# Optimization experiments

Measured on AMD Instinct MI355X. Metric: run time of the kernel, lower is better.

Reference implementation:

```python
import jax, jax.numpy as jnp
import numpy as np

NUM_CLASSES = 3
POS_T, NEG_T = 0.5, 0.3
RATIO = 3
W_OBJ, W_CLS, W_LOC = 1.0, 1.0, 2.0


def _pairwise_iou(a, b):
    # a: [N,4] anchors, b: [G,4] gt boxes, xyxy
    ix1 = jnp.maximum(a[:, None, 0], b[None, :, 0])
    iy1 = jnp.maximum(a[:, None, 1], b[None, :, 1])
    ix2 = jnp.minimum(a[:, None, 2], b[None, :, 2])
    iy2 = jnp.minimum(a[:, None, 3], b[None, :, 3])
    inter = jnp.clip(ix2 - ix1, 0) * jnp.clip(iy2 - iy1, 0)
    area_a = (a[:, 2] - a[:, 0]) * (a[:, 3] - a[:, 1])
    area_b = (b[:, 2] - b[:, 0]) * (b[:, 3] - b[:, 1])
    union = area_a[:, None] + area_b[None, :] - inter
    return inter / jnp.maximum(union, 1e-9)


def _masked_mean(x, m):
    c = m.sum()
    return jnp.where(c > 0, (x * m).sum() / jnp.maximum(c, 1.0), 0.0)


def _per_image(pred, anc, ax, ay, aw, ah, boxes_gt, labels_gt):
    # pred: [N, 5+nc]; anc: [N,4]; boxes_gt: [G,4]; labels_gt: [G] in 1..nc
    iou = _pairwise_iou(anc, boxes_gt)              # [N, G]
    best = jnp.argmax(iou, axis=1)
    best_iou = jnp.max(iou, axis=1)
    pos = best_iou >= POS_T
    neg = best_iou < NEG_T
    mb = boxes_gt[best]                             # matched boxes [N,4]
    ml = labels_gt[best]                            # matched labels [N]
    obj_logit = pred[:, 4]
    cls_logit = pred[:, 5:]
    obj_t = pos.astype(pred.dtype)
    # BCEWithLogits (numerically stable)
    obj_loss = jnp.maximum(obj_logit, 0) - obj_logit * obj_t + jnp.log1p(jnp.exp(-jnp.abs(obj_logit)))
    # hard negative mining: top-(3*num_pos) detached obj losses among negatives
    num_pos = pos.sum()
    k = jnp.minimum(RATIO * num_pos, neg.sum())
    cand = jnp.where(neg, jax.lax.stop_gradient(obj_loss), -1.0)
    order = jnp.argsort(-cand)
    ranks = jnp.zeros_like(order).at[order].set(jnp.arange(order.shape[0], dtype=order.dtype))
    sel_neg = neg & (ranks < k)
    loss_obj = _masked_mean(obj_loss, (pos | sel_neg).astype(pred.dtype))
    # classification over positives, labels shifted to 0-based
    logp = jax.nn.log_softmax(cls_logit, axis=-1)
    tgt = jnp.clip(ml - 1, 0)
    ce = -jnp.take_along_axis(logp, tgt[:, None], axis=1)[:, 0]
    loss_cls = _masked_mean(ce, pos.astype(pred.dtype))
    # localization over positives: SmoothL1 on encoded offsets
    gx = (mb[:, 0] + mb[:, 2]) * 0.5
    gy = (mb[:, 1] + mb[:, 3]) * 0.5
    gw = jnp.maximum(mb[:, 2] - mb[:, 0], 1e-6)
    gh = jnp.maximum(mb[:, 3] - mb[:, 1], 1e-6)
    loc_tgt = jnp.stack([(gx - ax) / aw, (gy - ay) / ah,
                         jnp.log(gw / aw), jnp.log(gh / ah)], axis=1)
    d = pred[:, :4] - loc_tgt
    ad = jnp.abs(d)
    sl1 = jnp.where(ad < 1.0, 0.5 * d * d, ad - 0.5)  # [N,4]
    pm = pos.astype(pred.dtype)
    cnt = 4.0 * pm.sum()
    loss_loc = jnp.where(cnt > 0, (sl1 * pm[:, None]).sum() / jnp.maximum(cnt, 1.0), 0.0)
    return loss_obj, loss_cls, loss_loc


def _detection_loss(preds, ancs, gt_boxes, gt_labels):
    B = preds[0].shape[0]
    obj_s = 0.0
    cls_s = 0.0
    loc_s = 0.0
    for pred, anc in zip(preds, ancs):
        Bp, C, H, W = pred.shape
        p = jnp.transpose(pred, (0, 2, 3, 1)).reshape(Bp, -1, 5 + NUM_CLASSES)
        ax = (anc[:, 0] + anc[:, 2]) * 0.5
        ay = (anc[:, 1] + anc[:, 3]) * 0.5
        aw = jnp.maximum(anc[:, 2] - anc[:, 0], 1e-6)
        ah = jnp.maximum(anc[:, 3] - anc[:, 1], 1e-6)
        lo, lc, ll = jax.vmap(
            lambda pb, bb, lb: _per_image(pb, anc, ax, ay, aw, ah, bb, lb)
        )(p, gt_boxes, gt_labels)
        obj_s = obj_s + lo.sum()
        cls_s = cls_s + lc.sum()
        loc_s = loc_s + ll.sum()
    obj_m = obj_s / B
    cls_m = cls_s / B
    loc_m = loc_s / B
    total = W_OBJ * obj_m + W_CLS * cls_m + W_LOC * loc_m
    return total, obj_m, cls_m, loc_m


def setup_inputs() -> dict:
    key = jax.random.key(0)
    k = jax.random.split(key, 8)
    B, G, A = 32, 50, 3
    img = 512.0
    scales = [(128, 128), (64, 64), (32, 32)]
    C = A * (5 + NUM_CLASSES)  # 24

    def make_anchors(H, W):
        stride = img / H
        ys, xs = np.meshgrid(np.arange(H), np.arange(W), indexing="ij")
        cx = (xs + 0.5) * stride
        cy = (ys + 0.5) * stride
        per = []
        for s in (1.0, 1.5, 2.0):
            half = s * stride
            per.append(np.stack([cx - half, cy - half, cx + half, cy + half], axis=-1).reshape(-1, 4))
        b = np.stack(per, axis=1).reshape(-1, 4)  # [H*W*A, 4], A innermost
        return jnp.asarray(b, dtype=jnp.float32)

    preds = [jax.random.normal(k[i], (B, C, H, W), dtype=jnp.float32) for i, (H, W) in enumerate(scales)]
    ancs = [make_anchors(H, W) for (H, W) in scales]
    cx = jax.random.uniform(k[3], (B, G)) * 384.0 + 64.0
    cy = jax.random.uniform(k[4], (B, G)) * 384.0 + 64.0
    w = jax.random.uniform(k[5], (B, G)) * 112.0 + 16.0
    h = jax.random.uniform(k[6], (B, G)) * 112.0 + 16.0
    gt_boxes = jnp.stack([cx - w / 2, cy - h / 2, cx + w / 2, cy + h / 2], axis=-1).astype(jnp.float32)
    gt_labels = jax.random.randint(k[7], (B, G), 1, NUM_CLASSES + 1)
    return {"p0": preds[0], "p1": preds[1], "p2": preds[2],
            "a0": ancs[0], "a1": ancs[1], "a2": ancs[2],
            "gt_boxes": gt_boxes, "gt_labels": gt_labels}


def reference(p0, p1, p2, a0, a1, a2, gt_boxes, gt_labels):
    return _detection_loss([p0, p1, p2], [a0, a1, a2], gt_boxes, gt_labels)
```

## Files before the change

### kernel.cpp

```cpp
#include <hip/hip_runtime.h>

#define SLOT_U64     200
#define NBLOCKS      2688
#define NBINS        192
#define BIN_OFF      872
#define SUM_SCALE    33554432.0f
#define INV_SUM_SCALE (1.0f/33554432.0f)

__device__ __forceinline__ float sl1f(float d){
  float ad = fabsf(d); return ad < 1.f ? 0.5f*d*d : ad - 0.5f;
}

__global__ __launch_bounds__(256) void k_main(
    const float* __restrict__ p0, const float* __restrict__ p1, const float* __restrict__ p2,
    const float* __restrict__ gtb, const int* __restrict__ gtl,
    unsigned long long* __restrict__ ws64)
{
  const int id = blockIdx.x;
  int s, bIm, chunk, H, lw; const float* p;
  if (id < 2048){ s=0; H=128; lw=7; chunk=id>>5;            bIm=id&31;          p=p0; }
  else if (id < 2560){ s=1; H=64; lw=6; chunk=(id-2048)>>5; bIm=(id-2048)&31;   p=p1; }
  else {              s=2; H=32; lw=5; chunk=(id-2560)>>5;  bIm=(id-2560)&31;   p=p2; }
  const int W = H, HW = H*W;
  const float stride = 512.0f/(float)H;
  const int tid = threadIdx.x;

  __shared__ float4 sBox[52];
  __shared__ float  sArea[52], sGx[52], sGy[52], sGw[52], sGh[52];
  __shared__ int    sLbl[52];
  __shared__ int    sNk;
  __shared__ unsigned long long sH[NBINS];
  __shared__ float  sRF[3][4];
  __shared__ unsigned int sRU[4];

  if (tid < 64){
    const int ymin = (chunk*256)>>lw;
    const int rowc = 256>>lw;
    const float by1 = ((float)ymin+0.5f)*stride - 2.0f*stride;
    const float by2 = ((float)(ymin+rowc-1)+0.5f)*stride + 2.0f*stride;
    bool keep=false; float4 gb=make_float4(0,0,0,0); int lbl=0;
    if (tid < 50){
      gb  = *(const float4*)(gtb + ((size_t)bIm*50 + tid)*4);
      lbl = gtl[bIm*50 + tid];
      keep = (fminf(by2, gb.w) - fmaxf(by1, gb.y)) > 0.f;
    }
    unsigned long long m = __ballot(keep);
    if (keep){
      int idx = __popcll(m & ((1ull<<tid)-1ull));
      sBox[idx]=gb;
      sArea[idx]=(gb.z-gb.x)*(gb.w-gb.y);
      sGx[idx]=(gb.x+gb.z)*0.5f;  sGy[idx]=(gb.y+gb.w)*0.5f;
      sGw[idx]=fmaxf(gb.z-gb.x,1e-6f); sGh[idx]=fmaxf(gb.w-gb.y,1e-6f);
      sLbl[idx]=lbl;
    }
    if (tid==0) sNk = __popcll(m);
  }
  if (tid < NBINS) sH[tid]=0ull;
  __syncthreads();

  const int nk = sNk;
  const int hw  = chunk*256 + tid;
  const int hwW = chunk*256 + (tid & ~63);
  const int y = hw>>lw, x = hw&(W-1);
  const float cx = ((float)x+0.5f)*stride, cy = ((float)y+0.5f)*stride;

  const float* pb = p + (size_t)bIm*24*HW + hw;
  float xo[3];
  #pragma unroll
  for (int a=0;a<3;a++) xo[a] = pb[(size_t)(a*8+4)*HW];

  const int wxlo = (W >= 64) ? (hwW & (W-1)) : 0;
  const int wxhi = (W >= 64) ? (wxlo + 63)   : (W-1);
  const int wylo = hwW>>lw, wyhi = (hwW+63)>>lw;
  const float m2 = 2.0f*stride;
  const float wx1 = ((float)wxlo+0.5f)*stride - m2;
  const float wx2 = ((float)wxhi+0.5f)*stride + m2;
  const float wy1 = ((float)wylo+0.5f)*stride - m2;
  const float wy2 = ((float)wyhi+0.5f)*stride + m2;

  float half[3]; half[0]=stride; half[1]=1.5f*stride; half[2]=2.0f*stride;
  float areaA[3], bi[3], bu[3]; int bj[3];
  #pragma unroll
  for (int a=0;a<3;a++){
    const float aw = 2.0f*half[a];
    areaA[a]=aw*aw; bi[a]=0.f; bu[a]=1e-9f; bj[a]=0;
  }
  for (int j=0;j<nk;j++){
    const float4 gb = sBox[j];
    if (gb.x >= wx2 || gb.z <= wx1 || gb.y >= wy2 || gb.w <= wy1) continue;
    const float ar = sArea[j];
    #pragma unroll
    for (int a=0;a<3;a++){
      const float iy1 = fmaxf(cy-half[a], gb.y), iy2 = fminf(cy+half[a], gb.w);
      const float ih  = fmaxf(iy2-iy1, 0.f);
      const float ix1 = fmaxf(cx-half[a], gb.x), ix2 = fminf(cx+half[a], gb.z);
      const float iw  = fmaxf(ix2-ix1, 0.f);
      const float inter = iw*ih;
      const float un = areaA[a] + ar - inter;
      if (inter*bu[a] > bi[a]*un){ bi[a]=inter; bu[a]=un; bj[a]=j; }
    }
  }

  int accPN=0;
  float accObj=0.f, accCls=0.f, accLoc=0.f;
  #pragma unroll
  for (int a=0;a<3;a++){
    const bool pos = bi[a] >= 0.5f*bu[a];
    const bool neg = bi[a] < 0.3f*bu[a];
    if (pos || neg){
      float objl = fmaxf(xo[a],0.f) - (pos ? xo[a] : 0.f)
                 + __logf(1.f + __expf(-fabsf(xo[a])));
      objl = fmaxf(objl, 0.f);
      if (neg){
        accPN += (1<<16);
        const int bin = min(max((int)(__float_as_uint(objl)>>20) - BIN_OFF, 0), NBINS-1);
        const unsigned long long pack =
            (1ull<<48) | (unsigned long long)__float2uint_rn(objl * SUM_SCALE);
        atomicAdd(&sH[bin], pack);
      } else {
        accPN += 1; accObj += objl;
        const int jb = bj[a];
        const float aw = 2.0f*half[a];
        const float c0=pb[(size_t)(a*8+5)*HW], c1=pb[(size_t)(a*8+6)*HW], c2=pb[(size_t)(a*8+7)*HW];
        const float mm = fmaxf(fmaxf(c0,c1),c2);
        const float lse = mm + __logf(__expf(c0-mm)+__expf(c1-mm)+__expf(c2-mm));
        const int t = max(sLbl[jb]-1, 0);
        const float ct = (t==0)?c0 : (t==1)?c1 : c2;
        accCls += lse - ct;
        const float tx = (sGx[jb]-cx)/aw;
        const float ty = (sGy[jb]-cy)/aw;
        const float tw = __logf(sGw[jb]/aw);
        const float th = __logf(sGh[jb]/aw);
        accLoc += sl1f(pb[(size_t)(a*8+0)*HW]-tx) + sl1f(pb[(size_t)(a*8+1)*HW]-ty)
                + sl1f(pb[(size_t)(a*8+2)*HW]-tw) + sl1f(pb[(size_t)(a*8+3)*HW]-th);
      }
    }
  }

  #pragma unroll
  for (int o=32;o;o>>=1){
    accPN  += __shfl_down(accPN,o,64);
    accObj += __shfl_down(accObj,o,64);
    accCls += __shfl_down(accCls,o,64);
    accLoc += __shfl_down(accLoc,o,64);
  }
  if ((tid & 63)==0){
    const int w = tid>>6;
    sRU[w]=(unsigned)accPN;
    sRF[0][w]=accObj; sRF[1][w]=accCls; sRF[2][w]=accLoc;
  }
  __syncthreads();

  unsigned long long* slot = ws64 + (size_t)id*SLOT_U64;
  if (tid < NBINS) slot[tid] = sH[tid];
  if (tid==0){
    unsigned t=0; float ob=0,cl=0,lc=0;
    #pragma unroll
    for (int w=0;w<4;w++){ t+=sRU[w]; ob+=sRF[0][w]; cl+=sRF[1][w]; lc+=sRF[2][w]; }
    slot[192] = ((unsigned long long)(t & 0xFFFFu) << 32) | (unsigned long long)(t >> 16);
    slot[193] = (unsigned long long)__float_as_uint(ob);
    slot[194] = (unsigned long long)__float_as_uint(cl);
    slot[195] = (unsigned long long)__float_as_uint(lc);
  }
}

__global__ __launch_bounds__(256) void k_select(const unsigned long long* __restrict__ ws64,
                                                float* __restrict__ out){
  const int g = blockIdx.x, tid = threadIdx.x;
  const int s = g>>5, bIm = g&31;
  const int nb   = (s==0)?64:(s==1)?16:4;
  const int base = (s==0)?0:(s==1)?2048:2560;

  __shared__ unsigned long long sHm[NBINS];
  __shared__ unsigned int sPos, sNeg;
  __shared__ float sObj, sCls, sLoc;

  if (tid < NBINS){
    unsigned long long a0=0ull, a1=0ull;
    int b=0;
    for (; b+1<nb; b+=2){
      a0 += ws64[(size_t)(base + b*32 + bIm)*SLOT_U64 + tid];
      a1 += ws64[(size_t)(base + (b+1)*32 + bIm)*SLOT_U64 + tid];
    }
    if (b<nb) a0 += ws64[(size_t)(base + b*32 + bIm)*SLOT_U64 + tid];
    sHm[tid] = a0 + a1;
  } else if (tid < 196){
    const int j = tid - 192;
    if (j==0){
      unsigned long long t=0ull;
      for (int b=0;b<nb;b++) t += ws64[(size_t)(base + b*32 + bIm)*SLOT_U64 + 192];
      sPos = (unsigned)(t>>32); sNeg = (unsigned)(t & 0xFFFFFFFFull);
    } else {
      float f=0.f;
      for (int b=0;b<nb;b++)
        f += __uint_as_float((unsigned)ws64[(size_t)(base + b*32 + bIm)*SLOT_U64 + 192 + j]);
      if (j==1) sObj=f; else if (j==2) sCls=f; else sLoc=f;
    }
  }
  __syncthreads();
  if (tid >= 64) return;

  const int lane = tid;
  const int pos  = (int)sPos;
  const int negc = (int)sNeg;
  const int k = min(3*pos, negc);
  float selSum = 0.f;

  if (k > 0){
    unsigned int c[3]; float sm[3];
    #pragma unroll
    for (int j=0;j<3;j++){
      const unsigned long long d = sHm[lane*3+j];
      c[j]  = (unsigned int)(d>>48);
      sm[j] = (float)(d & 0xFFFFFFFFFFFFull) * INV_SUM_SCALE;
    }
    const unsigned int c3 = c[0]+c[1]+c[2];
    unsigned int incl = c3;
    #pragma unroll
    for (int off=1; off<64; off<<=1){
      unsigned int yv = __shfl_down(incl, off, 64);
      if (lane+off < 64) incl += yv;
    }
    const unsigned int excl = incl - c3;
    int   tieL = -1, rL = 0; float avgL = 0.f;
    const bool hit = (excl < (unsigned)k) && (incl >= (unsigned)k);
    if (hit){
      unsigned int cum = excl;
      #pragma unroll
      for (int j=2;j>=0;j--){
        const unsigned int cc = c[j];
        if (cum + cc >= (unsigned)k){
          tieL = lane*3+j; rL = (int)((unsigned)k - cum);
          avgL = sm[j]/(float)cc;
          break;
        }
        cum += cc;
      }
    }
    const unsigned long long hm = __ballot(hit);
    const int src = __ffsll((long long)hm) - 1;
    const int   tie = __shfl(tieL, src, 64);
    const int   r   = __shfl(rL,   src, 64);
    const float avg = __shfl(avgL, src, 64);
    float above = 0.f;
    #pragma unroll
    for (int j=0;j<3;j++) if (lane*3+j > tie) above += sm[j];
    #pragma unroll
    for (int o=32;o;o>>=1) above += __shfl_down(above,o,64);
    selSum = above + (float)r * avg;
  }
  if (lane==0){
    const int cObj = pos + k;
    const float lo = (cObj>0) ? (sObj+selSum)/(float)cObj : 0.f;
    const float lc = (pos>0)  ? sCls/(float)pos           : 0.f;
    const float ll = (pos>0)  ? sLoc/(float)(4*pos)       : 0.f;
    const float invB = 1.f/32.f;
    atomicAdd(out+0, (lo + lc + 2.f*ll)*invB);
    atomicAdd(out+1, lo*invB);
    atomicAdd(out+2, lc*invB);
    atomicAdd(out+3, ll*invB);
  }
}

extern "C" void kernel_launch(void* const* d_in, const int* in_sizes, int n_in,
                              void* d_out, int out_size, void* d_ws, size_t ws_size,
                              hipStream_t stream){
  if (ws_size < (size_t)NBLOCKS*SLOT_U64*8) return;
  const float* p0  = (const float*)d_in[0];
  const float* p1  = (const float*)d_in[1];
  const float* p2  = (const float*)d_in[2];
  const float* gtb = (const float*)d_in[6];
  const int*   gtl = (const int*)d_in[7];
  unsigned long long* ws64 = (unsigned long long*)d_ws;
  float* out = (float*)d_out;

  hipLaunchKernelGGL(k_main,   dim3(NBLOCKS), dim3(256), 0, stream, p0,p1,p2,gtb,gtl,ws64);
  hipLaunchKernelGGL(k_select, dim3(96),      dim3(256), 0, stream, ws64, out);
}
```

Baseline: 141.2 us.

## Process four rows per thread to cut block count and reuse x-overlap math

Each main-kernel block now covers 1024 anchor positions instead of 256, with each thread handling four rows spaced 256 positions apart. The x-direction intersection is computed once per GT box and reused across the four rows. This cuts block count by four, along with per-block GT filtering, histogram init and slot writes, and the number of slots k_select must reduce, whose loop is unrolled by four. The costs are a looser per-wave GT culling window (taller y-range, so more boxes are tested), more registers per thread, and fewer blocks to fill the GPU.

```diff
diff --git a/kernel.cpp b/kernel.cpp
--- a/kernel.cpp
+++ b/kernel.cpp
@@ -1,7 +1,7 @@
 #include <hip/hip_runtime.h>
 
 #define SLOT_U64     200
-#define NBLOCKS      2688
+#define NBLOCKS      672
 #define NBINS        192
 #define BIN_OFF      872
 #define SUM_SCALE    33554432.0f
@@ -18,9 +18,9 @@
 {
   const int id = blockIdx.x;
   int s, bIm, chunk, H, lw; const float* p;
-  if (id < 2048){ s=0; H=128; lw=7; chunk=id>>5;            bIm=id&31;          p=p0; }
-  else if (id < 2560){ s=1; H=64; lw=6; chunk=(id-2048)>>5; bIm=(id-2048)&31;   p=p1; }
-  else {              s=2; H=32; lw=5; chunk=(id-2560)>>5;  bIm=(id-2560)&31;   p=p2; }
+  if (id < 512){      s=0; H=128; lw=7; chunk=id>>5;         bIm=id&31;        p=p0; }
+  else if (id < 640){ s=1; H=64;  lw=6; chunk=(id-512)>>5;   bIm=(id-512)&31;  p=p1; }
+  else {              s=2; H=32;  lw=5; chunk=0;             bIm=(id-640)&31;  p=p2; }
   const int W = H, HW = H*W;
   const float stride = 512.0f/(float)H;
   const int tid = threadIdx.x;
@@ -33,9 +33,25 @@
   __shared__ float  sRF[3][4];
   __shared__ unsigned int sRU[4];
 
+  const int hw0 = chunk*1024 + tid;
+  const int y0 = hw0>>lw, x = hw0&(W-1);
+  const float cx  = ((float)x+0.5f)*stride;
+  const float dy  = (float)(256>>lw)*stride;
+  float cyr[4];
+  cyr[0] = ((float)y0+0.5f)*stride;
+  cyr[1] = cyr[0]+dy; cyr[2] = cyr[0]+2.f*dy; cyr[3] = cyr[0]+3.f*dy;
+
+  const float* pb = p + (size_t)bIm*24*HW + hw0;
+  float xo[4][3];
+  #pragma unroll
+  for (int a=0;a<3;a++){
+    #pragma unroll
+    for (int r=0;r<4;r++) xo[r][a] = pb[(size_t)(a*8+4)*HW + r*256];
+  }
+
   if (tid < 64){
-    const int ymin = (chunk*256)>>lw;
-    const int rowc = 256>>lw;
+    const int ymin = (chunk*1024)>>lw;
+    const int rowc = 1024>>lw;
     const float by1 = ((float)ymin+0.5f)*stride - 2.0f*stride;
     const float by2 = ((float)(ymin+rowc-1)+0.5f)*stride + 2.0f*stride;
     bool keep=false; float4 gb=make_float4(0,0,0,0); int lbl=0;
@@ -59,19 +75,11 @@
   __syncthreads();
 
   const int nk = sNk;
-  const int hw  = chunk*256 + tid;
-  const int hwW = chunk*256 + (tid & ~63);
-  const int y = hw>>lw, x = hw&(W-1);
-  const float cx = ((float)x+0.5f)*stride, cy = ((float)y+0.5f)*stride;
-
-  const float* pb = p + (size_t)bIm*24*HW + hw;
-  float xo[3];
-  #pragma unroll
-  for (int a=0;a<3;a++) xo[a] = pb[(size_t)(a*8+4)*HW];
+  const int hwW = chunk*1024 + (tid & ~63);
 
   const int wxlo = (W >= 64) ? (hwW & (W-1)) : 0;
   const int wxhi = (W >= 64) ? (wxlo + 63)   : (W-1);
-  const int wylo = hwW>>lw, wyhi = (hwW+63)>>lw;
+  const int wylo = hwW>>lw, wyhi = (hwW+768+63)>>lw;
   const float m2 = 2.0f*stride;
   const float wx1 = ((float)wxlo+0.5f)*stride - m2;
   const float wx2 = ((float)wxhi+0.5f)*stride + m2;
@@ -79,11 +87,13 @@
   const float wy2 = ((float)wyhi+0.5f)*stride + m2;
 
   float half[3]; half[0]=stride; half[1]=1.5f*stride; half[2]=2.0f*stride;
-  float areaA[3], bi[3], bu[3]; int bj[3];
+  float areaA[3], bi[4][3], bu[4][3]; int bj[4][3];
   #pragma unroll
   for (int a=0;a<3;a++){
     const float aw = 2.0f*half[a];
-    areaA[a]=aw*aw; bi[a]=0.f; bu[a]=1e-9f; bj[a]=0;
+    areaA[a]=aw*aw;
+    #pragma unroll
+    for (int r=0;r<4;r++){ bi[r][a]=0.f; bu[r][a]=1e-9f; bj[r][a]=0; }
   }
   for (int j=0;j<nk;j++){
     const float4 gb = sBox[j];
@@ -91,48 +101,56 @@
     const float ar = sArea[j];
     #pragma unroll
     for (int a=0;a<3;a++){
-      const float iy1 = fmaxf(cy-half[a], gb.y), iy2 = fminf(cy+half[a], gb.w);
-      const float ih  = fmaxf(iy2-iy1, 0.f);
       const float ix1 = fmaxf(cx-half[a], gb.x), ix2 = fminf(cx+half[a], gb.z);
       const float iw  = fmaxf(ix2-ix1, 0.f);
-      const float inter = iw*ih;
-      const float un = areaA[a] + ar - inter;
-      if (inter*bu[a] > bi[a]*un){ bi[a]=inter; bu[a]=un; bj[a]=j; }
+      #pragma unroll
+      for (int r=0;r<4;r++){
+        const float iy1 = fmaxf(cyr[r]-half[a], gb.y), iy2 = fminf(cyr[r]+half[a], gb.w);
+        const float ih  = fmaxf(iy2-iy1, 0.f);
+        const float inter = iw*ih;
+        const float un = areaA[a] + ar - inter;
+        if (inter*bu[r][a] > bi[r][a]*un){ bi[r][a]=inter; bu[r][a]=un; bj[r][a]=j; }
+      }
     }
   }
 
   int accPN=0;
   float accObj=0.f, accCls=0.f, accLoc=0.f;
   #pragma unroll
-  for (int a=0;a<3;a++){
-    const bool pos = bi[a] >= 0.5f*bu[a];
-    const bool neg = bi[a] < 0.3f*bu[a];
-    if (pos || neg){
-      float objl = fmaxf(xo[a],0.f) - (pos ? xo[a] : 0.f)
-                 + __logf(1.f + __expf(-fabsf(xo[a])));
-      objl = fmaxf(objl, 0.f);
-      if (neg){
-        accPN += (1<<16);
-        const int bin = min(max((int)(__float_as_uint(objl)>>20) - BIN_OFF, 0), NBINS-1);
-        const unsigned long long pack =
-            (1ull<<48) | (unsigned long long)__float2uint_rn(objl * SUM_SCALE);
-        atomicAdd(&sH[bin], pack);
-      } else {
-        accPN += 1; accObj += objl;
-        const int jb = bj[a];
-        const float aw = 2.0f*half[a];
-        const float c0=pb[(size_t)(a*8+5)*HW], c1=pb[(size_t)(a*8+6)*HW], c2=pb[(size_t)(a*8+7)*HW];
-        const float mm = fmaxf(fmaxf(c0,c1),c2);
-        const float lse = mm + __logf(__expf(c0-mm)+__expf(c1-mm)+__expf(c2-mm));
-        const int t = max(sLbl[jb]-1, 0);
-        const float ct = (t==0)?c0 : (t==1)?c1 : c2;
-        accCls += lse - ct;
-        const float tx = (sGx[jb]-cx)/aw;
-        const float ty = (sGy[jb]-cy)/aw;
-        const float tw = __logf(sGw[jb]/aw);
-        const float th = __logf(sGh[jb]/aw);
-        accLoc += sl1f(pb[(size_t)(a*8+0)*HW]-tx) + sl1f(pb[(size_t)(a*8+1)*HW]-ty)
-                + sl1f(pb[(size_t)(a*8+2)*HW]-tw) + sl1f(pb[(size_t)(a*8+3)*HW]-th);
+  for (int r=0;r<4;r++){
+    #pragma unroll
+    for (int a=0;a<3;a++){
+      const bool pos = bi[r][a] >= 0.5f*bu[r][a];
+      const bool neg = bi[r][a] < 0.3f*bu[r][a];
+      if (pos || neg){
+        const float xv = xo[r][a];
+        float objl = fmaxf(xv,0.f) - (pos ? xv : 0.f)
+                   + __logf(1.f + __expf(-fabsf(xv)));
+        objl = fmaxf(objl, 0.f);
+        if (neg){
+          accPN += (1<<16);
+          const int bin = min(max((int)(__float_as_uint(objl)>>20) - BIN_OFF, 0), NBINS-1);
+          const unsigned long long pack =
+              (1ull<<48) | (unsigned long long)__float2uint_rn(objl * SUM_SCALE);
+          atomicAdd(&sH[bin], pack);
+        } else {
+          accPN += 1; accObj += objl;
+          const int jb = bj[r][a];
+          const float aw = 2.0f*half[a];
+          const size_t o = (size_t)(r*256);
+          const float c0=pb[(size_t)(a*8+5)*HW+o], c1=pb[(size_t)(a*8+6)*HW+o], c2=pb[(size_t)(a*8+7)*HW+o];
+          const float mm = fmaxf(fmaxf(c0,c1),c2);
+          const float lse = mm + __logf(__expf(c0-mm)+__expf(c1-mm)+__expf(c2-mm));
+          const int t = max(sLbl[jb]-1, 0);
+          const float ct = (t==0)?c0 : (t==1)?c1 : c2;
+          accCls += lse - ct;
+          const float tx = (sGx[jb]-cx)/aw;
+          const float ty = (sGy[jb]-cyr[r])/aw;
+          const float tw = __logf(sGw[jb]/aw);
+          const float th = __logf(sGh[jb]/aw);
+          accLoc += sl1f(pb[(size_t)(a*8+0)*HW+o]-tx) + sl1f(pb[(size_t)(a*8+1)*HW+o]-ty)
+                  + sl1f(pb[(size_t)(a*8+2)*HW+o]-tw) + sl1f(pb[(size_t)(a*8+3)*HW+o]-th);
+        }
       }
     }
   }
@@ -168,22 +186,25 @@
                                                 float* __restrict__ out){
   const int g = blockIdx.x, tid = threadIdx.x;
   const int s = g>>5, bIm = g&31;
-  const int nb   = (s==0)?64:(s==1)?16:4;
-  const int base = (s==0)?0:(s==1)?2048:2560;
+  const int nb   = (s==0)?16:(s==1)?4:1;
+  const int base = (s==0)?0:(s==1)?512:640;
 
   __shared__ unsigned long long sHm[NBINS];
   __shared__ unsigned int sPos, sNeg;
   __shared__ float sObj, sCls, sLoc;
 
   if (tid < NBINS){
-    unsigned long long a0=0ull, a1=0ull;
+    unsigned long long a0=0ull,a1=0ull,a2=0ull,a3=0ull;
     int b=0;
-    for (; b+1<nb; b+=2){
+    for (; b+3<nb; b+=4){
+      a0 += ws64[(size_t)(base + (b  )*32 + bIm)*SLOT_U64 + tid];
+      a1 += ws64[(size_t)(base + (b+1)*32 + bIm)*SLOT_U64 + tid];
+      a2 += ws64[(size_t)(base + (b+2)*32 + bIm)*SLOT_U64 + tid];
+      a3 += ws64[(size_t)(base + (b+3)*32 + bIm)*SLOT_U64 + tid];
+    }
+    for (; b<nb; b++)
       a0 += ws64[(size_t)(base + b*32 + bIm)*SLOT_U64 + tid];
-      a1 += ws64[(size_t)(base + (b+1)*32 + bIm)*SLOT_U64 + tid];
-    }
-    if (b<nb) a0 += ws64[(size_t)(base + b*32 + bIm)*SLOT_U64 + tid];
-    sHm[tid] = a0 + a1;
+    sHm[tid] = (a0+a1)+(a2+a3);
   } else if (tid < 196){
     const int j = tid - 192;
     if (j==0){
```

After: 139.5 us. About the same (-1.2%).
